# Performance work log

Measured on AMD Instinct MI355X. Metric: run time of the kernel, lower is better.

## Reference

```python
import jax, jax.numpy as jnp
import numpy as np

L_OUTPUT = 1024  # SequenceDecoder l_output


def setup_inputs() -> dict:
    key = jax.random.key(0)
    k1, k2, k3 = jax.random.split(key, 3)
    B, L, D, DO = 16, 4096, 1024, 1024
    x = jax.random.normal(k1, (B, L, D), dtype=jnp.float32)
    # 0/1 padding-style mask; valid_length = mask.sum(axis=1)
    attention_mask = jax.random.randint(k2, (B, L), 0, 2, dtype=jnp.int32)
    # nn.Linear(d_model, d_output): weight (DO, D), bias (DO,)
    W = jax.random.normal(k3, (DO, D), dtype=jnp.float32) * (1.0 / np.sqrt(D))
    b = jnp.zeros((DO,), dtype=jnp.float32)
    return {"x": x, "attention_mask": attention_mask, "W": W, "b": b}


def _restrict_last(x, attention_mask, l_output):
    """Vectorized equivalent of the per-sample Python loop in mode='last':
    for each batch row i, take the LAST s_i = min(valid_len_i, l_output)
    elements of the full sequence, zero-padded at the tail to l_output.
    (When all s_i == l_output this matches x[:, -l_output:, :], which is the
    only case the original torch.stack-based loop handles without error.)"""
    B, L, D = x.shape
    valid = attention_mask.sum(axis=1)                    # (B,)
    s = jnp.minimum(valid, l_output)                      # (B,)
    j = jnp.arange(l_output)                              # (l_output,)
    idx = jnp.clip(L - s[:, None] + j[None, :], 0, L - 1) # (B, l_output)
    gathered = jnp.take_along_axis(x, idx[:, :, None], axis=1)  # (B, l_output, D)
    keep = (j[None, :] < s[:, None])[:, :, None]          # (B, l_output, 1)
    return jnp.where(keep, gathered, jnp.zeros((), dtype=x.dtype))


def reference(x, attention_mask, W, b):
    # mode='last' restrict, then output_transform = nn.Linear(d_model, d_output)
    restricted = _restrict_last(x, attention_mask, L_OUTPUT)  # (B, l_output, D)
    return jnp.einsum('bld,od->blo', restricted, W) + b       # (B, l_output, DO)
```

## Files before the change

kernel.cpp:

```cpp
#include <hip/hip_runtime.h>
#include <hip/hip_bf16.h>

#define L_SEQ   4096
#define D_IN    1024
#define N_BATCH 16
#define L_OUT   1024
#define D_OUT   1024
#define M_DIM   (N_BATCH * L_OUT)
#define K_DIM   D_IN

#define BM 256
#define BN 256
#define BK 64
#define NKT (K_DIM / BK)

typedef __attribute__((ext_vector_type(4))) float  f32x4;
typedef __attribute__((ext_vector_type(8))) __bf16 bf16x8;
typedef __attribute__((ext_vector_type(4))) __bf16 bf16x4;

#define WS_A_OFF 0u
#define WS_W_OFF (32u * 1024u * 1024u)
#define WS_S_OFF (WS_W_OFF + 2u * 1024u * 1024u)

__global__ __launch_bounds__(256) void mask_sum_kernel(
    const int* __restrict__ mask, int* __restrict__ s_out)
{
    const int b = blockIdx.x;
    const int t = threadIdx.x;
    const int* row = mask + (size_t)b * L_SEQ;

    int sum = 0;
#pragma unroll
    for (int i = 0; i < L_SEQ / 256; ++i) sum += row[t + i * 256];

#pragma unroll
    for (int off = 32; off > 0; off >>= 1) sum += __shfl_down(sum, off, 64);

    __shared__ int wsum[4];
    if ((t & 63) == 0) wsum[t >> 6] = sum;
    __syncthreads();
    if (t == 0) {
        int total = wsum[0] + wsum[1] + wsum[2] + wsum[3];
        s_out[b] = total < L_OUT ? total : L_OUT;
    }
}

__global__ __launch_bounds__(256) void convert_kernel(
    const float* __restrict__ x,
    const float* __restrict__ W,
    const int*   __restrict__ s_arr,
    __bf16* __restrict__ wsA,
    __bf16* __restrict__ wsW)
{
    const int cb = blockIdx.x;
    const int t  = threadIdx.x;
    const int e0 = t * 4;

    if (cb < M_DIM) {
        const int rid = (cb & 7) * 2048 + (cb >> 3);
        const int b = rid >> 10;
        const int j = rid & (L_OUT - 1);
        const int s = s_arr[b];
        const int rsw  = (rid & 7) << 3;
        const int dste = (e0 & ~63) | ((e0 & 63) ^ rsw);
        __bf16* dst = wsA + (size_t)rid * K_DIM + dste;
        if (j < s) {
            const float* src = x + ((size_t)b * L_SEQ + (L_SEQ - s + j)) * D_IN + e0;
            f32x4 v = *(const f32x4*)src;
            bf16x4 o = {(__bf16)v.x, (__bf16)v.y, (__bf16)v.z, (__bf16)v.w};
            *(bf16x4*)dst = o;
        } else {
            bf16x4 o = {(__bf16)0.f, (__bf16)0.f, (__bf16)0.f, (__bf16)0.f};
            *(bf16x4*)dst = o;
        }
    } else {
        const int n = cb - M_DIM;
        const int rsw  = (n & 7) << 3;
        const int dste = (e0 & ~63) | ((e0 & 63) ^ rsw);
        const float* src = W + (size_t)n * D_IN + e0;
        f32x4 v = *(const f32x4*)src;
        bf16x4 o = {(__bf16)v.x, (__bf16)v.y, (__bf16)v.z, (__bf16)v.w};
        *(bf16x4*)(wsW + (size_t)n * K_DIM + dste) = o;
    }
}

__device__ __forceinline__ void gload16(const __bf16* g, __bf16* l) {
    __builtin_amdgcn_global_load_lds(
        (const __attribute__((address_space(1))) void*)g,
        (__attribute__((address_space(3))) void*)l,
        16, 0, 0);
}

#define FENCE() asm volatile("" ::: "memory")

__global__ __launch_bounds__(512, 2) void gemm_kernel(
    const __bf16* __restrict__ A,
    const __bf16* __restrict__ Wb,
    const float*  __restrict__ bias,
    float* __restrict__ out)
{
    __shared__ __bf16 smem[2][2][BM * BK];

    const int t  = threadIdx.x;
    const int bx = blockIdx.x;
    const int vb = (bx & 7) * 32 + (bx >> 3);
    const int tile_n = vb & 3;
    const int tile_m = vb >> 2;
    const int m0 = tile_m * BM;
    const int n0 = tile_n * BN;
    const int lane = t & 63;
    const int wave = t >> 6;
    const int wm = wave >> 2;
    const int wn = wave & 3;

    const int srow = t >> 3;
    const int scol = (t & 7) * 8;
    const int sdst = (t & 7) * 8;

    const __bf16* Ag = A  + (size_t)m0 * K_DIM;
    const __bf16* Bg = Wb + (size_t)n0 * K_DIM;

#define STAGE_HALF(gbase, lbase, h, kt_)                                   \
    {                                                                      \
        _Pragma("unroll")                                                  \
        for (int rd = 0; rd < 2; ++rd) {                                   \
            const int r_ = (h) * 128 + rd * 64 + srow;                     \
            gload16((gbase) + (size_t)r_ * K_DIM + (kt_) * BK + scol,      \
                    (lbase) + r_ * BK + sdst);                             \
        }                                                                  \
    }

    const int fr  = lane & 15;
    const int k8  = (lane >> 4) * 8;
    const int swz = (fr & 7) << 3;
    const int kc0 = k8 ^ swz;
    const int kc1 = (32 + k8) ^ swz;

    float bias_v[4];
#pragma unroll
    for (int g = 0; g < 4; ++g)
        bias_v[g] = bias[n0 + wn * 64 + g * 16 + fr];

    bf16x8 aF[4][2], bF0[2][2], bF1[2][2];
    f32x4 acc[8][4];
#pragma unroll
    for (int f = 0; f < 8; ++f)
#pragma unroll
        for (int g = 0; g < 4; ++g) acc[f][g] = (f32x4){0.f, 0.f, 0.f, 0.f};

#define LOAD_AF(Ac, mh)                                                    \
    {                                                                      \
        const __bf16* rb_ = (Ac) + (wm * 128 + (mh) * 64 + fr) * BK;       \
        _Pragma("unroll")                                                  \
        for (int i = 0; i < 4; ++i) {                                      \
            aF[i][0] = *(const bf16x8*)&rb_[i * 16 * BK + kc0];            \
            aF[i][1] = *(const bf16x8*)&rb_[i * 16 * BK + kc1];            \
        }                                                                  \
    }

#define LOAD_BF(Bc, nh, bF)                                                \
    {                                                                      \
        const __bf16* rb_ = (Bc) + (wn * 64 + (nh) * 32 + fr) * BK;        \
        _Pragma("unroll")                                                  \
        for (int j = 0; j < 2; ++j) {                                      \
            bF[j][0] = *(const bf16x8*)&rb_[j * 16 * BK + kc0];            \
            bF[j][1] = *(const bf16x8*)&rb_[j * 16 * BK + kc1];            \
        }                                                                  \
    }

#define MFMA_QUAD(mh, nh, bF)                                              \
    {                                                                      \
        _Pragma("unroll")                                                  \
        for (int i = 0; i < 4; ++i)                                        \
            _Pragma("unroll")                                              \
            for (int j = 0; j < 2; ++j) {                                  \
                f32x4 c_ = acc[(mh) * 4 + i][(nh) * 2 + j];                \
                c_ = __builtin_amdgcn_mfma_f32_16x16x32_bf16(              \
                    aF[i][0], bF[j][0], c_, 0, 0, 0);                      \
                c_ = __builtin_amdgcn_mfma_f32_16x16x32_bf16(              \
                    aF[i][1], bF[j][1], c_, 0, 0, 0);                      \
                acc[(mh) * 4 + i][(nh) * 2 + j] = c_;                      \
            }                                                              \
    }

    {
        __bf16* A0l = &smem[0][0][0];
        __bf16* B0l = &smem[0][1][0];
        __bf16* A1l = &smem[1][0][0];
        __bf16* B1l = &smem[1][1][0];
        STAGE_HALF(Ag, A0l, 0, 0);
        STAGE_HALF(Bg, B0l, 1, 0);
        STAGE_HALF(Ag, A0l, 1, 0);
        STAGE_HALF(Bg, B0l, 0, 0);
        STAGE_HALF(Ag, A1l, 0, 1);
        STAGE_HALF(Bg, B1l, 1, 1);
    }

    for (int kt = 0; kt < NKT; ++kt) {
        const int cur = kt & 1;
        __bf16* Ac = &smem[cur][0][0];
        __bf16* Bc = &smem[cur][1][0];
        __bf16* An = &smem[cur ^ 1][0][0];
        __bf16* Bn = &smem[cur ^ 1][1][0];

        FENCE();
        if (kt == NKT - 1) asm volatile("s_waitcnt vmcnt(0)" ::: "memory");
        else               asm volatile("s_waitcnt vmcnt(4)" ::: "memory");
        __builtin_amdgcn_s_barrier();
        FENCE();
        LOAD_AF(Ac, 0);
        LOAD_BF(Bc, 0, bF0);
        if (kt + 1 < NKT) {
            STAGE_HALF(Ag, An, 1, kt + 1);
            STAGE_HALF(Bg, Bn, 0, kt + 1);
        }
        asm volatile("s_waitcnt lgkmcnt(0)" ::: "memory");
        __builtin_amdgcn_sched_barrier(0);
        __builtin_amdgcn_s_setprio(1);
        MFMA_QUAD(0, 0, bF0);
        __builtin_amdgcn_s_setprio(0);

        FENCE();
        __builtin_amdgcn_s_barrier();
        FENCE();
        LOAD_BF(Bc, 1, bF1);
        asm volatile("s_waitcnt lgkmcnt(0)" ::: "memory");
        __builtin_amdgcn_sched_barrier(0);
        __builtin_amdgcn_s_setprio(1);
        MFMA_QUAD(0, 1, bF1);
        __builtin_amdgcn_s_setprio(0);

        FENCE();
        __builtin_amdgcn_s_barrier();
        FENCE();
        LOAD_AF(Ac, 1);
        if (kt + 2 < NKT) STAGE_HALF(Ag, Ac, 0, kt + 2);
        asm volatile("s_waitcnt lgkmcnt(0)" ::: "memory");
        __builtin_amdgcn_sched_barrier(0);
        __builtin_amdgcn_s_setprio(1);
        MFMA_QUAD(1, 1, bF1);
        __builtin_amdgcn_s_setprio(0);

        FENCE();
        __builtin_amdgcn_s_barrier();
        FENCE();
        if (kt + 2 < NKT) STAGE_HALF(Bg, Bc, 1, kt + 2);
        __builtin_amdgcn_s_setprio(1);
        MFMA_QUAD(1, 0, bF0);
        __builtin_amdgcn_s_setprio(0);
    }

    const int row0 = m0 + wm * 128 + (lane >> 4) * 4;
    const int col0 = n0 + wn * 64 + fr;
#pragma unroll
    for (int f = 0; f < 8; ++f)
#pragma unroll
        for (int g = 0; g < 4; ++g)
#pragma unroll
            for (int rr = 0; rr < 4; ++rr)
                out[(size_t)(row0 + f * 16 + rr) * D_OUT + (col0 + g * 16)] =
                    acc[f][g][rr] + bias_v[g];

#undef STAGE_HALF
#undef LOAD_AF
#undef LOAD_BF
#undef MFMA_QUAD
}

extern "C" void kernel_launch(void* const* d_in, const int* in_sizes, int n_in,
                              void* d_out, int out_size, void* d_ws, size_t ws_size,
                              hipStream_t stream) {
    const float* x    = (const float*)d_in[0];
    const int*   mask = (const int*)d_in[1];
    const float* W    = (const float*)d_in[2];
    const float* bias = (const float*)d_in[3];
    float*       out  = (float*)d_out;

    __bf16* wsA   = (__bf16*)((char*)d_ws + WS_A_OFF);
    __bf16* wsW   = (__bf16*)((char*)d_ws + WS_W_OFF);
    int*    s_arr = (int*)((char*)d_ws + WS_S_OFF);

    mask_sum_kernel<<<dim3(N_BATCH), dim3(256), 0, stream>>>(mask, s_arr);

    convert_kernel<<<dim3(M_DIM + D_OUT), dim3(256), 0, stream>>>(
        x, W, s_arr, wsA, wsW);

    const int grid = (M_DIM / BM) * (D_OUT / BN);
    gemm_kernel<<<dim3(grid), dim3(512), 0, stream>>>(wsA, wsW, bias, out);
}
```

Baseline: 61.47 us.

## Load all LDS fragments upfront per k-tile and drop intermediate lgkmcnt waits

Reads all A and B register fragments for the current k-tile from shared memory at the start of the iteration, using separate aF0/aF1 buffers. This lets the explicit lgkmcnt waits and sched barriers between MFMA quads be removed. The intent is to overlap LDS reads with MFMA work and cut stalls, at the cost of more vector registers for the duplicated A fragments. Register pressure may rise enough to hurt occupancy or cause spills.

New measurement: 64.06 us. 4.2% more time.

```diff
diff --git a/kernel.cpp b/kernel.cpp
--- a/kernel.cpp
+++ b/kernel.cpp
@@ -115,7 +115,6 @@
 
     const int srow = t >> 3;
     const int scol = (t & 7) * 8;
-    const int sdst = (t & 7) * 8;
 
     const __bf16* Ag = A  + (size_t)m0 * K_DIM;
     const __bf16* Bg = Wb + (size_t)n0 * K_DIM;
@@ -126,7 +125,7 @@
         for (int rd = 0; rd < 2; ++rd) {                                   \
             const int r_ = (h) * 128 + rd * 64 + srow;                     \
             gload16((gbase) + (size_t)r_ * K_DIM + (kt_) * BK + scol,      \
-                    (lbase) + r_ * BK + sdst);                             \
+                    (lbase) + r_ * BK + scol);                             \
         }                                                                  \
     }
 
@@ -141,20 +140,20 @@
     for (int g = 0; g < 4; ++g)
         bias_v[g] = bias[n0 + wn * 64 + g * 16 + fr];
 
-    bf16x8 aF[4][2], bF0[2][2], bF1[2][2];
+    bf16x8 aF0[4][2], aF1[4][2], bF0[2][2], bF1[2][2];
     f32x4 acc[8][4];
 #pragma unroll
     for (int f = 0; f < 8; ++f)
 #pragma unroll
         for (int g = 0; g < 4; ++g) acc[f][g] = (f32x4){0.f, 0.f, 0.f, 0.f};
 
-#define LOAD_AF(Ac, mh)                                                    \
+#define LOAD_AF(AF, Ac, mh)                                                \
     {                                                                      \
         const __bf16* rb_ = (Ac) + (wm * 128 + (mh) * 64 + fr) * BK;       \
         _Pragma("unroll")                                                  \
         for (int i = 0; i < 4; ++i) {                                      \
-            aF[i][0] = *(const bf16x8*)&rb_[i * 16 * BK + kc0];            \
-            aF[i][1] = *(const bf16x8*)&rb_[i * 16 * BK + kc1];            \
+            AF[i][0] = *(const bf16x8*)&rb_[i * 16 * BK + kc0];            \
+            AF[i][1] = *(const bf16x8*)&rb_[i * 16 * BK + kc1];            \
         }                                                                  \
     }
 
@@ -168,7 +167,7 @@
         }                                                                  \
     }
 
-#define MFMA_QUAD(mh, nh, bF)                                              \
+#define MFMA_QUAD(AF, mh, nh, bF)                                          \
     {                                                                      \
         _Pragma("unroll")                                                  \
         for (int i = 0; i < 4; ++i)                                        \
@@ -176,9 +175,9 @@
             for (int j = 0; j < 2; ++j) {                                  \
                 f32x4 c_ = acc[(mh) * 4 + i][(nh) * 2 + j];                \
                 c_ = __builtin_amdgcn_mfma_f32_16x16x32_bf16(              \
-                    aF[i][0], bF[j][0], c_, 0, 0, 0);                      \
+                    AF[i][0], bF[j][0], c_, 0, 0, 0);                      \
                 c_ = __builtin_amdgcn_mfma_f32_16x16x32_bf16(              \
-                    aF[i][1], bF[j][1], c_, 0, 0, 0);                      \
+                    AF[i][1], bF[j][1], c_, 0, 0, 0);                      \
                 acc[(mh) * 4 + i][(nh) * 2 + j] = c_;                      \
             }                                                              \
     }
@@ -208,37 +207,31 @@
         else               asm volatile("s_waitcnt vmcnt(4)" ::: "memory");
         __builtin_amdgcn_s_barrier();
         FENCE();
-        LOAD_AF(Ac, 0);
+        LOAD_AF(aF0, Ac, 0);
         LOAD_BF(Bc, 0, bF0);
+        LOAD_BF(Bc, 1, bF1);
+        LOAD_AF(aF1, Ac, 1);
         if (kt + 1 < NKT) {
             STAGE_HALF(Ag, An, 1, kt + 1);
             STAGE_HALF(Bg, Bn, 0, kt + 1);
         }
-        asm volatile("s_waitcnt lgkmcnt(0)" ::: "memory");
-        __builtin_amdgcn_sched_barrier(0);
-        __builtin_amdgcn_s_setprio(1);
-        MFMA_QUAD(0, 0, bF0);
-        __builtin_amdgcn_s_setprio(0);
-
-        FENCE();
-        __builtin_amdgcn_s_barrier();
-        FENCE();
-        LOAD_BF(Bc, 1, bF1);
-        asm volatile("s_waitcnt lgkmcnt(0)" ::: "memory");
-        __builtin_amdgcn_sched_barrier(0);
-        __builtin_amdgcn_s_setprio(1);
-        MFMA_QUAD(0, 1, bF1);
-        __builtin_amdgcn_s_setprio(0);
-
-        FENCE();
-        __builtin_amdgcn_s_barrier();
-        FENCE();
-        LOAD_AF(Ac, 1);
+        __builtin_amdgcn_s_setprio(1);
+        MFMA_QUAD(aF0, 0, 0, bF0);
+        __builtin_amdgcn_s_setprio(0);
+
+        FENCE();
+        __builtin_amdgcn_s_barrier();
+        FENCE();
+        __builtin_amdgcn_s_setprio(1);
+        MFMA_QUAD(aF0, 0, 1, bF1);
+        __builtin_amdgcn_s_setprio(0);
+
+        FENCE();
+        __builtin_amdgcn_s_barrier();
+        FENCE();
         if (kt + 2 < NKT) STAGE_HALF(Ag, Ac, 0, kt + 2);
-        asm volatile("s_waitcnt lgkmcnt(0)" ::: "memory");
-        __builtin_amdgcn_sched_barrier(0);
-        __builtin_amdgcn_s_setprio(1);
-        MFMA_QUAD(1, 1, bF1);
+        __builtin_amdgcn_s_setprio(1);
+        MFMA_QUAD(aF1, 1, 1, bF1);
         __builtin_amdgcn_s_setprio(0);
 
         FENCE();
@@ -246,7 +239,7 @@
         FENCE();
         if (kt + 2 < NKT) STAGE_HALF(Bg, Bc, 1, kt + 2);
         __builtin_amdgcn_s_setprio(1);
-        MFMA_QUAD(1, 0, bF0);
+        MFMA_QUAD(aF1, 1, 0, bF0);
         __builtin_amdgcn_s_setprio(0);
     }
 
```

## Fuse x gather and bf16 conversion into GEMM prologue, merge mask-sum with W convert

Applied to the files above, without the earlier changes.

The separate x gather/convert pass is removed. Each GEMM workgroup now gathers its own 256 rows of x, converts them to bf16 and writes them, swizzled, into the workspace before starting the K loop. The mask-sum and W-conversion kernels are merged into one prep kernel, which cuts one launch and the full-size intermediate conversion pass. In exchange, the four N-tile workgroups that share an M tile each redo the same gather and conversion. That multiplies x reads and workspace writes, and the conversion runs serially before any MFMA work.

Measured after the change: 68.95 us. 1.12x slower.

```diff
diff --git a/kernel.cpp b/kernel.cpp
--- a/kernel.cpp
+++ b/kernel.cpp
@@ -22,59 +22,31 @@
 #define WS_W_OFF (32u * 1024u * 1024u)
 #define WS_S_OFF (WS_W_OFF + 2u * 1024u * 1024u)
 
-__global__ __launch_bounds__(256) void mask_sum_kernel(
-    const int* __restrict__ mask, int* __restrict__ s_out)
-{
-    const int b = blockIdx.x;
-    const int t = threadIdx.x;
-    const int* row = mask + (size_t)b * L_SEQ;
-
-    int sum = 0;
-#pragma unroll
-    for (int i = 0; i < L_SEQ / 256; ++i) sum += row[t + i * 256];
-
-#pragma unroll
-    for (int off = 32; off > 0; off >>= 1) sum += __shfl_down(sum, off, 64);
-
-    __shared__ int wsum[4];
-    if ((t & 63) == 0) wsum[t >> 6] = sum;
-    __syncthreads();
-    if (t == 0) {
-        int total = wsum[0] + wsum[1] + wsum[2] + wsum[3];
-        s_out[b] = total < L_OUT ? total : L_OUT;
-    }
-}
-
-__global__ __launch_bounds__(256) void convert_kernel(
-    const float* __restrict__ x,
+__global__ __launch_bounds__(256) void prep_kernel(
+    const int*   __restrict__ mask,
     const float* __restrict__ W,
-    const int*   __restrict__ s_arr,
-    __bf16* __restrict__ wsA,
+    int*    __restrict__ s_out,
     __bf16* __restrict__ wsW)
 {
-    const int cb = blockIdx.x;
-    const int t  = threadIdx.x;
-    const int e0 = t * 4;
-
-    if (cb < M_DIM) {
-        const int rid = (cb & 7) * 2048 + (cb >> 3);
-        const int b = rid >> 10;
-        const int j = rid & (L_OUT - 1);
-        const int s = s_arr[b];
-        const int rsw  = (rid & 7) << 3;
-        const int dste = (e0 & ~63) | ((e0 & 63) ^ rsw);
-        __bf16* dst = wsA + (size_t)rid * K_DIM + dste;
-        if (j < s) {
-            const float* src = x + ((size_t)b * L_SEQ + (L_SEQ - s + j)) * D_IN + e0;
-            f32x4 v = *(const f32x4*)src;
-            bf16x4 o = {(__bf16)v.x, (__bf16)v.y, (__bf16)v.z, (__bf16)v.w};
-            *(bf16x4*)dst = o;
-        } else {
-            bf16x4 o = {(__bf16)0.f, (__bf16)0.f, (__bf16)0.f, (__bf16)0.f};
-            *(bf16x4*)dst = o;
+    const int t = threadIdx.x;
+    if (blockIdx.x < 16) {
+        const int b = blockIdx.x;
+        const int* row = mask + (size_t)b * L_SEQ;
+        int sum = 0;
+#pragma unroll
+        for (int i = 0; i < L_SEQ / 256; ++i) sum += row[t + i * 256];
+#pragma unroll
+        for (int off = 32; off > 0; off >>= 1) sum += __shfl_down(sum, off, 64);
+        __shared__ int wsum[4];
+        if ((t & 63) == 0) wsum[t >> 6] = sum;
+        __syncthreads();
+        if (t == 0) {
+            int total = wsum[0] + wsum[1] + wsum[2] + wsum[3];
+            s_out[b] = total < L_OUT ? total : L_OUT;
         }
     } else {
-        const int n = cb - M_DIM;
+        const int n  = blockIdx.x - 16;
+        const int e0 = t * 4;
         const int rsw  = (n & 7) << 3;
         const int dste = (e0 & ~63) | ((e0 & 63) ^ rsw);
         const float* src = W + (size_t)n * D_IN + e0;
@@ -94,9 +66,11 @@
 #define FENCE() asm volatile("" ::: "memory")
 
 __global__ __launch_bounds__(512, 2) void gemm_kernel(
-    const __bf16* __restrict__ A,
+    const float*  __restrict__ x,
     const __bf16* __restrict__ Wb,
     const float*  __restrict__ bias,
+    const int*    __restrict__ s_arr,
+    __bf16*       __restrict__ wsA,
     float* __restrict__ out)
 {
     __shared__ __bf16 smem[2][2][BM * BK];
@@ -113,12 +87,42 @@
     const int wm = wave >> 2;
     const int wn = wave & 3;
 
+    {
+        const int bb = m0 >> 10;
+        const int s  = s_arr[bb];
+        const int jb = m0 & (L_OUT - 1);
+        const float* xb = x + ((size_t)bb * L_SEQ + (size_t)(L_SEQ - s)) * D_IN;
+        __bf16* wA = wsA + (size_t)m0 * K_DIM;
+        const int rset = t >> 7;
+        const int cg   = (t & 127) * 8;
+        const bf16x8 zo = {(__bf16)0.f, (__bf16)0.f, (__bf16)0.f, (__bf16)0.f,
+                           (__bf16)0.f, (__bf16)0.f, (__bf16)0.f, (__bf16)0.f};
+#pragma unroll 4
+        for (int sw = 0; sw < 64; ++sw) {
+            const int r = rset + sw * 4;
+            const int j = jb + r;
+            const int dste = (cg & ~63) | ((cg & 63) ^ ((r & 7) << 3));
+            __bf16* dst = wA + (size_t)r * K_DIM + dste;
+            if (j < s) {
+                const float* src = xb + (size_t)j * D_IN + cg;
+                f32x4 v0 = *(const f32x4*)(src);
+                f32x4 v1 = *(const f32x4*)(src + 4);
+                bf16x8 o = {(__bf16)v0.x, (__bf16)v0.y, (__bf16)v0.z, (__bf16)v0.w,
+                            (__bf16)v1.x, (__bf16)v1.y, (__bf16)v1.z, (__bf16)v1.w};
+                *(bf16x8*)dst = o;
+            } else {
+                *(bf16x8*)dst = zo;
+            }
+        }
+        asm volatile("s_waitcnt vmcnt(0)" ::: "memory");
+        __builtin_amdgcn_s_barrier();
+    }
+
     const int srow = t >> 3;
     const int scol = (t & 7) * 8;
-    const int sdst = (t & 7) * 8;
-
-    const __bf16* Ag = A  + (size_t)m0 * K_DIM;
-    const __bf16* Bg = Wb + (size_t)n0 * K_DIM;
+
+    const __bf16* Ag = wsA + (size_t)m0 * K_DIM;
+    const __bf16* Bg = Wb  + (size_t)n0 * K_DIM;
 
 #define STAGE_HALF(gbase, lbase, h, kt_)                                   \
     {                                                                      \
@@ -126,7 +130,7 @@
         for (int rd = 0; rd < 2; ++rd) {                                   \
             const int r_ = (h) * 128 + rd * 64 + srow;                     \
             gload16((gbase) + (size_t)r_ * K_DIM + (kt_) * BK + scol,      \
-                    (lbase) + r_ * BK + sdst);                             \
+                    (lbase) + r_ * BK + scol);                             \
         }                                                                  \
     }
 
@@ -280,11 +284,10 @@
     __bf16* wsW   = (__bf16*)((char*)d_ws + WS_W_OFF);
     int*    s_arr = (int*)((char*)d_ws + WS_S_OFF);
 
-    mask_sum_kernel<<<dim3(N_BATCH), dim3(256), 0, stream>>>(mask, s_arr);
-
-    convert_kernel<<<dim3(M_DIM + D_OUT), dim3(256), 0, stream>>>(
-        x, W, s_arr, wsA, wsW);
+    prep_kernel<<<dim3(16 + D_OUT), dim3(256), 0, stream>>>(
+        mask, W, s_arr, wsW);
 
     const int grid = (M_DIM / BM) * (D_OUT / BN);
-    gemm_kernel<<<dim3(grid), dim3(512), 0, stream>>>(wsA, wsW, bias, out);
-}
+    gemm_kernel<<<dim3(grid), dim3(512), 0, stream>>>(
+        x, wsW, bias, s_arr, wsA, out);
+}
```
